# Kernel tuning notes

Measured on AMD Instinct MI355X. Metric: run time of the kernel, lower is better.

Reference implementation:

```python
import jax, jax.numpy as jnp
import numpy as np
from jax.scipy.special import logsumexp

B, S, T = 128, 2048, 64


def setup_inputs() -> dict:
    key = jax.random.key(0)
    k_em, k_tags, k_tr, k_st, k_en = jax.random.split(key, 5)
    emissions = jax.random.normal(k_em, (B, S, T), dtype=jnp.float32)
    tags = jax.random.randint(k_tags, (B, S), 0, T, dtype=jnp.int32)
    mask = jnp.ones((B, S), dtype=jnp.bool_)
    transitions = jax.random.normal(k_tr, (T, T), dtype=jnp.float32)
    start_transitions = jax.random.normal(k_st, (T,), dtype=jnp.float32)
    end_transitions = jax.random.normal(k_en, (T,), dtype=jnp.float32)
    return {"emissions": emissions, "tags": tags, "mask": mask,
            "transitions": transitions, "start_transitions": start_transitions,
            "end_transitions": end_transitions}


def _compute_score(emissions, tags, mask, transitions, start_t, end_t):
    # emissions: (B,S,T), tags: (B,S), mask: (B,S) bool
    maskf = mask.astype(emissions.dtype)
    # emission score at the gold tag per step: (B,S)
    emit = jnp.take_along_axis(emissions, tags[..., None], axis=2)[..., 0]
    # NOTE: source uses transitions[curr_tags, prev_tags]
    trans = transitions[tags[:, 1:], tags[:, :-1]]  # (B,S-1)
    score = start_t[tags[:, 0]] + emit[:, 0]
    score = score + jnp.sum((trans + emit[:, 1:]) * maskf[:, 1:], axis=1)
    last_idx = jnp.sum(mask.astype(jnp.int32), axis=1) - 1  # (B,)
    last_tags = jnp.take_along_axis(tags, last_idx[:, None], axis=1)[:, 0]
    return score + end_t[last_tags]


def _compute_partition(emissions, mask, transitions, end_t, start_t):
    # forward algorithm as a scan; alpha: (B,T)
    alpha0 = start_t + emissions[:, 0]

    def step(alpha, inp):
        em_t, m_t = inp  # (B,T), (B,)
        # next_alpha[b,j] = logsumexp_i alpha[b,i] + transitions[i,j] + em_t[b,j]
        next_alpha = logsumexp(alpha[:, :, None] + transitions[None], axis=1) + em_t
        alpha = jnp.where(m_t[:, None], next_alpha, alpha)
        return alpha, None

    ems = jnp.swapaxes(emissions[:, 1:], 0, 1)  # (S-1,B,T)
    ms = jnp.swapaxes(mask[:, 1:], 0, 1)        # (S-1,B)
    alpha, _ = jax.lax.scan(step, alpha0, (ems, ms))
    return logsumexp(alpha + end_t, axis=1)


def reference(emissions, tags, mask, transitions, start_transitions, end_transitions):
    score = _compute_score(emissions, tags, mask, transitions, start_transitions, end_transitions)
    partition = _compute_partition(emissions, mask, transitions, end_transitions, start_transitions)
    return -(score - partition).mean()
```

## Files before the change

kernel.cpp:

```cpp
#include <hip/hip_runtime.h>
#include <hip/hip_bf16.h>

#define TT 64
#define SS 2048
#define BB 128
#define CC 16
#define LL (SS / CC)
#define PAN 2
#define PCOLS 32
#define CSTRIDE 136

using bf16x8 = __attribute__((ext_vector_type(8))) short;
using f32x4  = __attribute__((ext_vector_type(4))) float;

union B8u { uint4 u; bf16x8 v; };

__device__ __forceinline__ float fexp2(float x) { return __builtin_amdgcn_exp2f(x); }
__device__ __forceinline__ float flog2(float x) { return __builtin_amdgcn_logf(x); }
__device__ __forceinline__ float fexp(float x)  { return fexp2(x * 1.4426950408889634f); }

__device__ __forceinline__ float wave_max(float v) {
#pragma unroll
    for (int off = 32; off > 0; off >>= 1) v = fmaxf(v, __shfl_xor(v, off, 64));
    return v;
}

__device__ __forceinline__ float wave_sum(float v) {
#pragma unroll
    for (int off = 32; off > 0; off >>= 1) v += __shfl_xor(v, off, 64);
    return v;
}

__device__ __forceinline__ unsigned pack_bf16(float lo, float hi) {
    return __builtin_amdgcn_perm(__float_as_uint(hi), __float_as_uint(lo), 0x07060302u);
}

__global__ __launch_bounds__(64, 4) void crf_chunk_kernel(
    const float* __restrict__ emissions,
    const float* __restrict__ transitions,
    __hip_bfloat16* __restrict__ Ms,
    float* __restrict__ Mbase)
{
    const int blk = blockIdx.x;
    const int p = blk & 1;
    const int c = (blk >> 1) & (CC - 1);
    const int b = blk >> 5;
    const int l = threadIdx.x;
    const int c16 = l & 15, q = l >> 4;
    const float LOG2E = 1.4426950408889634f;

    __shared__ __align__(16) unsigned char sbuf[PCOLS * CSTRIDE];
    __shared__ __align__(16) float xbuf[2][TT];

    bf16x8 A[4][2];
#pragma unroll
    for (int mt = 0; mt < 4; ++mt)
#pragma unroll
        for (int kt = 0; kt < 2; ++kt) {
            const int row = mt * 16 + c16;
#pragma unroll
            for (int jj = 0; jj < 8; ++jj) {
                const int k = kt * 32 + q * 8 + jj;
                float e = fexp(transitions[k * TT + row]);
                A[mt][kt][jj] = (short)(__float_as_uint(e) >> 16);
            }
        }

    const int t0 = (c == 0) ? 1 : c * LL;
    const int t1 = c * LL + LL - 1;
    const float* emb = emissions + (size_t)b * SS * TT;

    {
        int* ib = (int*)sbuf;
#pragma unroll
        for (int i = l; i < PCOLS * CSTRIDE / 4; i += 64) ib[i] = 0;
        asm volatile("" ::: "memory");
        if (l < PCOLS)
            *(unsigned short*)(sbuf + l * CSTRIDE + (p * PCOLS + l) * 2) = 0x3F80;
        xbuf[t0 & 1][l] = fexp2(emb[(size_t)t0 * TT + l] * LOG2E);
        asm volatile("" ::: "memory");
    }

    float base = 0.f;

#define CRF_STEP(T, RENORM)                                                   \
    {                                                                         \
        const int tcur = (T);                                                 \
        const int tp = tcur + 1 > t1 ? t1 : tcur + 1;                         \
        float emN = emb[(size_t)tp * TT + l];                                 \
        B8u Bf[2][2];                                           \
        _Pragma("unroll")                                                     \
        for (int kt = 0; kt < 2; ++kt)                                        \
            _Pragma("unroll")                                                 \
            for (int nt = 0; nt < 2; ++nt) {                                  \
                const unsigned char* pb = sbuf + (nt * 16 + c16) * CSTRIDE + kt * 64 + q * 16; \
                uint2 lo = *(const uint2*)pb;                                 \
                uint2 hi = *(const uint2*)(pb + 8);                           \
                Bf[kt][nt].u = make_uint4(lo.x, lo.y, hi.x, hi.y);            \
            }                                                                 \
        f32x4 xvv[4];                                                         \
        _Pragma("unroll")                                                     \
        for (int mt = 0; mt < 4; ++mt)                                        \
            xvv[mt] = *(const f32x4*)&xbuf[tcur & 1][mt * 16 + q * 4];        \
        f32x4 D[4][2];                                                        \
        __builtin_amdgcn_s_setprio(1);                                        \
        _Pragma("unroll")                                                     \
        for (int mt = 0; mt < 4; ++mt)                                        \
            _Pragma("unroll")                                                 \
            for (int nt = 0; nt < 2; ++nt) {                                  \
                f32x4 z = {0.f, 0.f, 0.f, 0.f};                               \
                z = __builtin_amdgcn_mfma_f32_16x16x32_bf16(A[mt][0], Bf[0][nt].v, z, 0, 0, 0); \
                z = __builtin_amdgcn_mfma_f32_16x16x32_bf16(A[mt][1], Bf[1][nt].v, z, 0, 0, 0); \
                D[mt][nt] = z;                                                \
            }                                                                 \
        __builtin_amdgcn_s_setprio(0);                                        \
        xbuf[(tcur + 1) & 1][l] = fexp2(emN * LOG2E);    \
        if (RENORM) {                                                         \
             \
             \
            unsigned mb = (unsigned)__builtin_amdgcn_readfirstlane(           \
                (int)__float_as_uint(D[0][0][0]));                            \
            int e = (int)(mb >> 23) - 126 + 8;                                \
            float s = __uint_as_float((unsigned)(127 - e) << 23);   \
            base += (float)e;                                                 \
            _Pragma("unroll")                                                 \
            for (int mt = 0; mt < 4; ++mt) xvv[mt] *= s;                      \
        }                                                                     \
        _Pragma("unroll")                                                     \
        for (int mt = 0; mt < 4; ++mt)                                        \
            _Pragma("unroll")                                                 \
            for (int nt = 0; nt < 2; ++nt) {                                  \
                f32x4 prod = D[mt][nt] * xvv[mt];                             \
                uint2 w;                                                      \
                w.x = pack_bf16(prod[0], prod[1]);                            \
                w.y = pack_bf16(prod[2], prod[3]);                            \
                *(uint2*)(sbuf + (nt * 16 + c16) * CSTRIDE + mt * 32 + q * 8) = w; \
            }                                                                 \
        asm volatile("" ::: "memory");         \
    }

    int t = t0;
    while (t & 3) {
        CRF_STEP(t, ((t & 3) == 3));
        ++t;
    }
    for (; t <= t1; t += 4) {
        CRF_STEP(t, 0);
        CRF_STEP(t + 1, 0);
        CRF_STEP(t + 2, 0);
        CRF_STEP(t + 3, 1);
    }
#undef CRF_STEP

    {
        unsigned* op = (unsigned*)(Ms + (size_t)blk * 2048 + (size_t)l * PCOLS);
#pragma unroll
        for (int i2 = 0; i2 < 16; ++i2) {
            unsigned short s0 = *(const unsigned short*)(sbuf + (2 * i2) * CSTRIDE + l * 2);
            unsigned short s1 = *(const unsigned short*)(sbuf + (2 * i2 + 1) * CSTRIDE + l * 2);
            op[i2] = (unsigned)s0 | ((unsigned)s1 << 16);
        }
        if (l == 0) Mbase[blk] = base;
    }
}

__global__ __launch_bounds__(256) void crf_fused_tail(
    const float* __restrict__ emissions,
    const int* __restrict__ tags,
    const float* __restrict__ transitions,
    const float* __restrict__ start_t,
    const float* __restrict__ end_t,
    const __hip_bfloat16* __restrict__ Ms,
    const float* __restrict__ Mbase,
    float* __restrict__ out)
{
    const int b = blockIdx.x;
    const int tid = threadIdx.x;
    const int wv = tid >> 6;
    const int j = tid & 63;
    const float LOG2E = 1.4426950408889634f;
    const float LN2   = 0.6931471805599453f;
    __shared__ __align__(16) float pbuf[TT];
    __shared__ float red[4];
    __shared__ float bred[4];

    uint4 m[4 * PAN];
    float bp[PAN];
    {
        const int pbase = (b * CC + wv) * PAN;
        const uint4* src = (const uint4*)(Ms + (size_t)pbase * 2048) + j * 4;
#pragma unroll
        for (int pp = 0; pp < PAN; ++pp) {
#pragma unroll
            for (int d = 0; d < 4; ++d) m[4 * pp + d] = src[pp * 256 + d];
            bp[pp] = Mbase[pbase + pp];
        }
    }

    const int* tg = tags + b * SS;
    const float* em = emissions + (size_t)b * SS * TT;
    {
        const int s0 = tid * 8;
        int4 ta = *(const int4*)(tg + s0);
        int4 tb = *(const int4*)(tg + s0 + 4);
        int t_[8] = {ta.x, ta.y, ta.z, ta.w, tb.x, tb.y, tb.z, tb.w};
        float acc = 0.f;
#pragma unroll
        for (int u = 0; u < 8; ++u) acc += em[(s0 + u) * TT + t_[u]];
#pragma unroll
        for (int u = 1; u < 8; ++u) acc += transitions[t_[u] * TT + t_[u - 1]];
        if (tid > 0) acc += transitions[t_[0] * TT + tg[s0 - 1]];
        if (tid == 0) acc += start_t[t_[0]];
        if (tid == 255) acc += end_t[t_[7]];
        acc = wave_sum(acc);
        if (j == 0) red[wv] = acc;
    }

    float btot = 0.f;
    if (wv == 0) {
        float r2 = (start_t[j] + em[j]) * LOG2E;
        float m2 = wave_max(r2);
        btot = m2;
        pbuf[j] = fexp2(r2 - m2);
    }
    __syncthreads();

    for (int cch = 0; cch < CC; ++cch) {
        if (wv == (cch & 3)) {
            float bmax = fmaxf(bp[0], bp[1]);
            float acc = 0.f;
#pragma unroll
            for (int pp = 0; pp < PAN; ++pp) {
                float dot = 0.f;
#pragma unroll
                for (int d = 0; d < 4; ++d) {
                    uint4 u4 = m[4 * pp + d];
                    const float* pb = pbuf + pp * PCOLS + d * 8;
                    unsigned uu[4] = {u4.x, u4.y, u4.z, u4.w};
#pragma unroll
                    for (int k = 0; k < 4; ++k) {
                        dot = fmaf(__uint_as_float(uu[k] << 16), pb[2 * k], dot);
                        dot = fmaf(__uint_as_float(uu[k] & 0xFFFF0000u), pb[2 * k + 1], dot);
                    }
                }
                acc = fmaf(fexp2(bp[pp] - bmax), dot, acc);
            }
            float mv = wave_max(acc);
            float v = acc / mv;
            btot += bmax + flog2(mv);
            const int nch = cch + 4;
            if (nch < CC) {
                const int pbase = (b * CC + nch) * PAN;
                const uint4* src = (const uint4*)(Ms + (size_t)pbase * 2048) + j * 4;
#pragma unroll
                for (int pp = 0; pp < PAN; ++pp) {
#pragma unroll
                    for (int d = 0; d < 4; ++d) m[4 * pp + d] = src[pp * 256 + d];
                    bp[pp] = Mbase[pbase + pp];
                }
            }
            pbuf[j] = v;
        }
        __syncthreads();
    }

    if (j == 0) bred[wv] = btot;
    __syncthreads();

    if (wv == 0) {
        float v = pbuf[j];
        float w = v * fexp(end_t[j]);
        float s = wave_sum(w);
        if (j == 0) {
            float Btot = (bred[0] + bred[1]) + (bred[2] + bred[3]);
            float partition = LN2 * (Btot + flog2(s));
            float score = (red[0] + red[1]) + (red[2] + red[3]);
            atomicAdd(out, (partition - score) * (1.0f / BB));
        }
    }
}

__global__ __launch_bounds__(256) void crf_score_kernel(
    const float* __restrict__ emissions,
    const int* __restrict__ tags,
    const float* __restrict__ transitions,
    const float* __restrict__ start_t,
    const float* __restrict__ end_t,
    float* __restrict__ score)
{
    const int b = blockIdx.x;
    const int tid = threadIdx.x;
    const int* tg = tags + b * SS;
    const float* em = emissions + (size_t)b * SS * TT;
    const int s0 = tid * 8;
    int4 ta = *(const int4*)(tg + s0);
    int4 tb = *(const int4*)(tg + s0 + 4);
    int t_[8] = {ta.x, ta.y, ta.z, ta.w, tb.x, tb.y, tb.z, tb.w};
    float acc = 0.f;
#pragma unroll
    for (int u = 0; u < 8; ++u) acc += em[(s0 + u) * TT + t_[u]];
#pragma unroll
    for (int u = 1; u < 8; ++u) acc += transitions[t_[u] * TT + t_[u - 1]];
    if (tid > 0) acc += transitions[t_[0] * TT + tg[s0 - 1]];
    if (tid == 0) acc += start_t[t_[0]];
    if (tid == 255) acc += end_t[t_[7]];
    acc = wave_sum(acc);
    __shared__ float red[4];
    if ((tid & 63) == 0) red[tid >> 6] = acc;
    __syncthreads();
    if (tid == 0) score[b] = (red[0] + red[1]) + (red[2] + red[3]);
}

__global__ __launch_bounds__(64, 1) void crf_partition_seq(
    const float* __restrict__ emissions,
    const float* __restrict__ transitions,
    const float* __restrict__ start_t,
    const float* __restrict__ end_t,
    float* __restrict__ partition)
{
    const int b = blockIdx.x;
    const int j = threadIdx.x;
    const float LOG2E = 1.4426950408889634f;
    const float LN2   = 0.6931471805599453f;
    const float* em = emissions + (size_t)b * SS * TT;
    __shared__ __align__(16) float pbuf[TT];

    float E[TT];
#pragma unroll
    for (int k = 0; k < TT; ++k)
        E[k] = fexp2(transitions[k * TT + j] * LOG2E);

    float r = (start_t[j] + em[j]) * LOG2E;
    float base;
    { float m = wave_max(r); base = m; r -= m; }

    for (int t = 1; t < SS; ++t) {
        float emv = em[t * TT + j];
        float p = fexp2(r);
        pbuf[j] = p;
        asm volatile("" ::: "memory");
        float a0 = 0.f, a1 = 0.f, a2 = 0.f, a3 = 0.f;
        const float4* pb4 = (const float4*)pbuf;
#pragma unroll
        for (int cc = 0; cc < 16; ++cc) {
            float4 pv = pb4[cc];
            a0 = fmaf(pv.x, E[4 * cc + 0], a0);
            a1 = fmaf(pv.y, E[4 * cc + 1], a1);
            a2 = fmaf(pv.z, E[4 * cc + 2], a2);
            a3 = fmaf(pv.w, E[4 * cc + 3], a3);
        }
        asm volatile("" ::: "memory");
        r = fmaf(emv, LOG2E, flog2((a0 + a1) + (a2 + a3)));
        if ((t & 3) == 3) { float m = wave_max(r); base += m; r -= m; }
    }
    float v = fmaf(end_t[j], LOG2E, r);
    float m = wave_max(v);
    float s = wave_sum(fexp2(v - m));
    if (j == 0) partition[b] = LN2 * (base + m + flog2(s));
}

__global__ __launch_bounds__(128) void crf_final_kernel(
    const float* __restrict__ partition,
    const float* __restrict__ score,
    float* __restrict__ out)
{
    const int i = threadIdx.x;
    float d = partition[i] - score[i];
#pragma unroll
    for (int off = 32; off > 0; off >>= 1) d += __shfl_xor(d, off, 64);
    __shared__ float red[2];
    if ((i & 63) == 0) red[i >> 6] = d;
    __syncthreads();
    if (i == 0) out[0] = (red[0] + red[1]) * (1.0f / BB);
}

extern "C" void kernel_launch(void* const* d_in, const int* in_sizes, int n_in,
                              void* d_out, int out_size, void* d_ws, size_t ws_size,
                              hipStream_t stream) {
    const float* emissions   = (const float*)d_in[0];
    const int*   tags        = (const int*)d_in[1];
    const float* transitions = (const float*)d_in[3];
    const float* start_t     = (const float*)d_in[4];
    const float* end_t       = (const float*)d_in[5];

    const int NPANEL = BB * CC * PAN;
    const size_t MS_BYTES = (size_t)NPANEL * 2048 * 2;
    unsigned char* w = (unsigned char*)d_ws;
    __hip_bfloat16* Ms = (__hip_bfloat16*)w;
    float* Mbase       = (float*)(w + MS_BYTES);
    const size_t need  = MS_BYTES + NPANEL * sizeof(float);

    if (ws_size >= need) {
        hipMemsetAsync(d_out, 0, sizeof(float), stream);
        crf_chunk_kernel<<<NPANEL, 64, 0, stream>>>(emissions, transitions, Ms, Mbase);
        crf_fused_tail<<<BB, 256, 0, stream>>>(emissions, tags, transitions,
                                               start_t, end_t, Ms, Mbase, (float*)d_out);
    } else {
        float* p2 = (float*)d_ws;
        float* sc = p2 + BB;
        crf_partition_seq<<<BB, 64, 0, stream>>>(emissions, transitions, start_t, end_t, p2);
        crf_score_kernel<<<BB, 256, 0, stream>>>(emissions, tags, transitions, start_t, end_t, sc);
        crf_final_kernel<<<1, 128, 0, stream>>>(p2, sc, (float*)d_out);
    }
}
```

Baseline: 239.5 us.

## Keep chunk transfer-matrix state in MFMA registers instead of LDS round-trip

Switches from 16x16x32 bf16 MFMA to 16x16x16 bf16 MFMA, whose output fragment layout matches the B-operand layout, so the running product stays in registers each step. This removes the per-step LDS write and read of the B panel and the initial LDS zeroing. It doubles the MFMA instruction count per step (narrower K) and adds an f16 fallback path with different renormalisation frequency.

```diff
diff --git a/kernel.cpp b/kernel.cpp
--- a/kernel.cpp
+++ b/kernel.cpp
@@ -1,5 +1,6 @@
 #include <hip/hip_runtime.h>
 #include <hip/hip_bf16.h>
+#include <hip/hip_fp16.h>
 
 #define TT 64
 #define SS 2048
@@ -10,10 +11,9 @@
 #define PCOLS 32
 #define CSTRIDE 136
 
-using bf16x8 = __attribute__((ext_vector_type(8))) short;
+using bf16x4 = __attribute__((ext_vector_type(4))) short;
+using f16x4  = __attribute__((ext_vector_type(4))) _Float16;
 using f32x4  = __attribute__((ext_vector_type(4))) float;
-
-union B8u { uint4 u; bf16x8 v; };
 
 __device__ __forceinline__ float fexp2(float x) { return __builtin_amdgcn_exp2f(x); }
 __device__ __forceinline__ float flog2(float x) { return __builtin_amdgcn_logf(x); }
@@ -34,6 +34,33 @@
 __device__ __forceinline__ unsigned pack_bf16(float lo, float hi) {
     return __builtin_amdgcn_perm(__float_as_uint(hi), __float_as_uint(lo), 0x07060302u);
 }
+
+__device__ __forceinline__ unsigned pack_f16(float lo, float hi) {
+    auto h = __builtin_amdgcn_cvt_pkrtz(lo, hi);
+    union { decltype(h) v; unsigned u; } cv;
+    cv.v = h;
+    return cv.u;
+}
+
+#if !defined(__HIP_DEVICE_COMPILE__) || __has_builtin(__builtin_amdgcn_mfma_f32_16x16x16bf16_1k)
+  #define USE_BF16 1
+  #define RPER 4
+  #define ONE16 0x3F80u
+  typedef bf16x4 abfrag;
+  #define MFMA16(A, B, C) __builtin_amdgcn_mfma_f32_16x16x16bf16_1k((A), (B), (C), 0, 0, 0)
+  #define PK(lo, hi) pack_bf16((lo), (hi))
+#elif __has_builtin(__builtin_amdgcn_mfma_f32_16x16x16f16)
+  #define USE_BF16 0
+  #define RPER 2
+  #define ONE16 0x3C00u
+  typedef f16x4 abfrag;
+  #define MFMA16(A, B, C) __builtin_amdgcn_mfma_f32_16x16x16f16((A), (B), (C), 0, 0, 0)
+  #define PK(lo, hi) pack_f16((lo), (hi))
+#else
+  #error "no 16x16x16 mfma available"
+#endif
+
+union Bu { uint2 u; abfrag v; };
 
 __global__ __launch_bounds__(64, 4) void crf_chunk_kernel(
     const float* __restrict__ emissions,
@@ -52,34 +79,42 @@
     __shared__ __align__(16) unsigned char sbuf[PCOLS * CSTRIDE];
     __shared__ __align__(16) float xbuf[2][TT];
 
-    bf16x8 A[4][2];
+    abfrag A[4][4];
 #pragma unroll
     for (int mt = 0; mt < 4; ++mt)
 #pragma unroll
-        for (int kt = 0; kt < 2; ++kt) {
+        for (int kt = 0; kt < 4; ++kt) {
             const int row = mt * 16 + c16;
 #pragma unroll
-            for (int jj = 0; jj < 8; ++jj) {
-                const int k = kt * 32 + q * 8 + jj;
+            for (int jj = 0; jj < 4; ++jj) {
+                const int k = kt * 16 + q * 4 + jj;
                 float e = fexp(transitions[k * TT + row]);
+#if USE_BF16
                 A[mt][kt][jj] = (short)(__float_as_uint(e) >> 16);
+#else
+                A[mt][kt][jj] = (_Float16)e;
+#endif
             }
+        }
+
+    Bu Bfr[4][2];
+#pragma unroll
+    for (int kt = 0; kt < 4; ++kt)
+#pragma unroll
+        for (int nt = 0; nt < 2; ++nt) {
+            const int gcol = p * 32 + nt * 16 + c16;
+            const int r0 = kt * 16 + q * 4;
+            unsigned d0 = (r0 + 0 == gcol ? ONE16 : 0u) | ((r0 + 1 == gcol ? ONE16 : 0u) << 16);
+            unsigned d1 = (r0 + 2 == gcol ? ONE16 : 0u) | ((r0 + 3 == gcol ? ONE16 : 0u) << 16);
+            Bfr[kt][nt].u = make_uint2(d0, d1);
         }
 
     const int t0 = (c == 0) ? 1 : c * LL;
     const int t1 = c * LL + LL - 1;
     const float* emb = emissions + (size_t)b * SS * TT;
 
-    {
-        int* ib = (int*)sbuf;
-#pragma unroll
-        for (int i = l; i < PCOLS * CSTRIDE / 4; i += 64) ib[i] = 0;
-        asm volatile("" ::: "memory");
-        if (l < PCOLS)
-            *(unsigned short*)(sbuf + l * CSTRIDE + (p * PCOLS + l) * 2) = 0x3F80;
-        xbuf[t0 & 1][l] = fexp2(emb[(size_t)t0 * TT + l] * LOG2E);
-        asm volatile("" ::: "memory");
-    }
+    xbuf[t0 & 1][l] = fexp2(emb[(size_t)t0 * TT + l] * LOG2E);
+    asm volatile("" ::: "memory");
 
     float base = 0.f;
 
@@ -88,16 +123,6 @@
         const int tcur = (T);                                                 \
         const int tp = tcur + 1 > t1 ? t1 : tcur + 1;                         \
         float emN = emb[(size_t)tp * TT + l];                                 \
-        B8u Bf[2][2];                                           \
-        _Pragma("unroll")                                                     \
-        for (int kt = 0; kt < 2; ++kt)                                        \
-            _Pragma("unroll")                                                 \
-            for (int nt = 0; nt < 2; ++nt) {                                  \
-                const unsigned char* pb = sbuf + (nt * 16 + c16) * CSTRIDE + kt * 64 + q * 16; \
-                uint2 lo = *(const uint2*)pb;                                 \
-                uint2 hi = *(const uint2*)(pb + 8);                           \
-                Bf[kt][nt].u = make_uint4(lo.x, lo.y, hi.x, hi.y);            \
-            }                                                                 \
         f32x4 xvv[4];                                                         \
         _Pragma("unroll")                                                     \
         for (int mt = 0; mt < 4; ++mt)                                        \
@@ -109,12 +134,15 @@
             _Pragma("unroll")                                                 \
             for (int nt = 0; nt < 2; ++nt) {                                  \
                 f32x4 z = {0.f, 0.f, 0.f, 0.f};                               \
-                z = __builtin_amdgcn_mfma_f32_16x16x32_bf16(A[mt][0], Bf[0][nt].v, z, 0, 0, 0); \
-                z = __builtin_amdgcn_mfma_f32_16x16x32_bf16(A[mt][1], Bf[1][nt].v, z, 0, 0, 0); \
+                z = MFMA16(A[mt][0], Bfr[0][nt].v, z);                        \
+                z = MFMA16(A[mt][1], Bfr[1][nt].v, z);                        \
+                z = MFMA16(A[mt][2], Bfr[2][nt].v, z);                        \
+                z = MFMA16(A[mt][3], Bfr[3][nt].v, z);                        \
                 D[mt][nt] = z;                                                \
             }                                                                 \
         __builtin_amdgcn_s_setprio(0);                                        \
-        xbuf[(tcur + 1) & 1][l] = fexp2(emN * LOG2E);    \
+        xbuf[(tcur + 1) & 1][l] = fexp2(emN * LOG2E);                         \
+        asm volatile("" ::: "memory");                                        \
         if (RENORM) {                                                         \
              \
              \
@@ -131,28 +159,50 @@
             _Pragma("unroll")                                                 \
             for (int nt = 0; nt < 2; ++nt) {                                  \
                 f32x4 prod = D[mt][nt] * xvv[mt];                             \
-                uint2 w;                                                      \
-                w.x = pack_bf16(prod[0], prod[1]);                            \
-                w.y = pack_bf16(prod[2], prod[3]);                            \
-                *(uint2*)(sbuf + (nt * 16 + c16) * CSTRIDE + mt * 32 + q * 8) = w; \
+                Bfr[mt][nt].u.x = PK(prod[0], prod[1]);                       \
+                Bfr[mt][nt].u.y = PK(prod[2], prod[3]);                       \
             }                                                                 \
-        asm volatile("" ::: "memory");         \
     }
 
     int t = t0;
-    while (t & 3) {
-        CRF_STEP(t, ((t & 3) == 3));
+    while (t & (RPER - 1)) {
+        CRF_STEP(t, ((t & (RPER - 1)) == RPER - 1));
         ++t;
     }
-    for (; t <= t1; t += 4) {
+    for (; t <= t1; t += RPER) {
+#if RPER == 4
         CRF_STEP(t, 0);
         CRF_STEP(t + 1, 0);
         CRF_STEP(t + 2, 0);
         CRF_STEP(t + 3, 1);
+#else
+        CRF_STEP(t, 0);
+        CRF_STEP(t + 1, 1);
+#endif
     }
 #undef CRF_STEP
 
     {
+#pragma unroll
+        for (int kt = 0; kt < 4; ++kt)
+#pragma unroll
+            for (int nt = 0; nt < 2; ++nt) {
+                unsigned d0 = Bfr[kt][nt].u.x;
+                unsigned d1 = Bfr[kt][nt].u.y;
+#if !USE_BF16
+                {
+                    float l0 = __half2float(__ushort_as_half((unsigned short)(d0 & 0xFFFF)));
+                    float h0 = __half2float(__ushort_as_half((unsigned short)(d0 >> 16)));
+                    float l1 = __half2float(__ushort_as_half((unsigned short)(d1 & 0xFFFF)));
+                    float h1 = __half2float(__ushort_as_half((unsigned short)(d1 >> 16)));
+                    d0 = pack_bf16(l0, h0);
+                    d1 = pack_bf16(l1, h1);
+                }
+#endif
+                unsigned char* cbase = sbuf + (nt * 16 + c16) * CSTRIDE + (kt * 16 + q * 4) * 2;
+                *(uint2*)cbase = make_uint2(d0, d1);
+            }
+        asm volatile("" ::: "memory");
         unsigned* op = (unsigned*)(Ms + (size_t)blk * 2048 + (size_t)l * PCOLS);
 #pragma unroll
         for (int i2 = 0; i2 < 16; ++i2) {
@@ -391,7 +441,7 @@
     const size_t need  = MS_BYTES + NPANEL * sizeof(float);
 
     if (ws_size >= need) {
-        hipMemsetAsync(d_out, 0, sizeof(float), stream);
+        (void)hipMemsetAsync(d_out, 0, sizeof(float), stream);
         crf_chunk_kernel<<<NPANEL, 64, 0, stream>>>(emissions, transitions, Ms, Mbase);
         crf_fused_tail<<<BB, 256, 0, stream>>>(emissions, tags, transitions,
                                                start_t, end_t, Ms, Mbase, (float*)d_out);
```

Result: slower. 264.3 us (+10.4%).

## Keep recurrence state in registers using 32x32 MFMA and permlane32 swaps

Applied to the files above, without the earlier changes.

Each chunk step now uses 32x32x16 bf16 MFMAs instead of 16x16x32 ones, with the transition matrix laid out to match. The running product matrix stays in registers as the B operand, and the output-to-input layout change is done with permlane32_swap rather than a round trip through LDS. This removes per-step LDS writes and reads and their latency from the serial dependency chain. The cost is a more intricate lane permutation, including a runtime flip probe, and a shuffle fallback when the builtin is missing.

```diff
diff --git a/kernel.cpp b/kernel.cpp
--- a/kernel.cpp
+++ b/kernel.cpp
@@ -1,5 +1,6 @@
 #include <hip/hip_runtime.h>
 #include <hip/hip_bf16.h>
+#include <hip/hip_fp16.h>
 
 #define TT 64
 #define SS 2048
@@ -9,11 +10,11 @@
 #define PAN 2
 #define PCOLS 32
 #define CSTRIDE 136
+#define RPER 4
 
 using bf16x8 = __attribute__((ext_vector_type(8))) short;
 using f32x4  = __attribute__((ext_vector_type(4))) float;
-
-union B8u { uint4 u; bf16x8 v; };
+using f32x16 = __attribute__((ext_vector_type(16))) float;
 
 __device__ __forceinline__ float fexp2(float x) { return __builtin_amdgcn_exp2f(x); }
 __device__ __forceinline__ float flog2(float x) { return __builtin_amdgcn_logf(x); }
@@ -33,6 +34,40 @@
 
 __device__ __forceinline__ unsigned pack_bf16(float lo, float hi) {
     return __builtin_amdgcn_perm(__float_as_uint(hi), __float_as_uint(lo), 0x07060302u);
+}
+
+#if !defined(__HIP_DEVICE_COMPILE__) || __has_builtin(__builtin_amdgcn_permlane32_swap)
+#define HAVE_PLSWAP 1
+#else
+#define HAVE_PLSWAP 0
+#endif
+
+__device__ __forceinline__ void plswap2(unsigned &x, unsigned &y) {
+#if HAVE_PLSWAP
+    static_assert(sizeof(__builtin_amdgcn_permlane32_swap(0, 0, false, false)) == 8,
+                  "permlane32_swap must return two dwords");
+    auto pr = __builtin_amdgcn_permlane32_swap((int)x, (int)y, false, false);
+    x = (unsigned)((int*)&pr)[0];
+    y = (unsigned)((int*)&pr)[1];
+#else
+    const int h = (int)((threadIdx.x >> 5) & 1);
+    unsigned sx = (unsigned)__shfl_xor((int)x, 32, 64);
+    unsigned sy = (unsigned)__shfl_xor((int)y, 32, 64);
+    unsigned nx = h ? sy : x;
+    unsigned ny = h ? y : sx;
+    x = nx; y = ny;
+#endif
+}
+
+__device__ __forceinline__ int plswap_flip() {
+#if HAVE_PLSWAP
+    int l = (int)threadIdx.x;
+    auto pr = __builtin_amdgcn_permlane32_swap(l, 1000 + l, false, false);
+    int r0 = ((int*)&pr)[0];
+    return (__builtin_amdgcn_readfirstlane(r0) != 0) ? 1 : 0;
+#else
+    return 0;
+#endif
 }
 
 __global__ __launch_bounds__(64, 4) void crf_chunk_kernel(
@@ -46,40 +81,48 @@
     const int c = (blk >> 1) & (CC - 1);
     const int b = blk >> 5;
     const int l = threadIdx.x;
-    const int c16 = l & 15, q = l >> 4;
+    const int n = l & 31;
+    const int h = l >> 5;
     const float LOG2E = 1.4426950408889634f;
 
     __shared__ __align__(16) unsigned char sbuf[PCOLS * CSTRIDE];
     __shared__ __align__(16) float xbuf[2][TT];
 
-    bf16x8 A[4][2];
-#pragma unroll
-    for (int mt = 0; mt < 4; ++mt)
-#pragma unroll
-        for (int kt = 0; kt < 2; ++kt) {
-            const int row = mt * 16 + c16;
+    const int flip = plswap_flip();
+
+    bf16x8 A[2][4];
+#pragma unroll
+    for (int mt = 0; mt < 2; ++mt)
+#pragma unroll
+        for (int kt = 0; kt < 4; ++kt) {
+            const int m = 32 * mt + n;
 #pragma unroll
             for (int jj = 0; jj < 8; ++jj) {
-                const int k = kt * 32 + q * 8 + jj;
-                float e = fexp(transitions[k * TT + row]);
+                const int d = jj >> 1;
+                const int k = 16 * kt + 8 * h + 2 * (d & 1) + 4 * ((d >> 1) ^ flip) + (jj & 1);
+                float e = fexp(transitions[k * TT + m]);
                 A[mt][kt][jj] = (short)(__float_as_uint(e) >> 16);
             }
+        }
+
+    union B8 { unsigned d[4]; bf16x8 v; } S[4];
+#pragma unroll
+    for (int kt = 0; kt < 4; ++kt)
+#pragma unroll
+        for (int d = 0; d < 4; ++d) {
+            const int R = 16 * kt + 8 * h + 2 * (d & 1) + 4 * ((d >> 1) ^ flip);
+            const int gcol = p * 32 + n;
+            unsigned lo = (R == gcol) ? 0x3F80u : 0u;
+            unsigned hi = (R + 1 == gcol) ? 0x3F80u : 0u;
+            S[kt].d[d] = lo | (hi << 16);
         }
 
     const int t0 = (c == 0) ? 1 : c * LL;
     const int t1 = c * LL + LL - 1;
     const float* emb = emissions + (size_t)b * SS * TT;
 
-    {
-        int* ib = (int*)sbuf;
-#pragma unroll
-        for (int i = l; i < PCOLS * CSTRIDE / 4; i += 64) ib[i] = 0;
-        asm volatile("" ::: "memory");
-        if (l < PCOLS)
-            *(unsigned short*)(sbuf + l * CSTRIDE + (p * PCOLS + l) * 2) = 0x3F80;
-        xbuf[t0 & 1][l] = fexp2(emb[(size_t)t0 * TT + l] * LOG2E);
-        asm volatile("" ::: "memory");
-    }
+    xbuf[t0 & 1][l] = fexp2(emb[(size_t)t0 * TT + l] * LOG2E);
+    asm volatile("" ::: "memory");
 
     float base = 0.f;
 
@@ -88,63 +131,64 @@
         const int tcur = (T);                                                 \
         const int tp = tcur + 1 > t1 ? t1 : tcur + 1;                         \
         float emN = emb[(size_t)tp * TT + l];                                 \
-        B8u Bf[2][2];                                           \
-        _Pragma("unroll")                                                     \
-        for (int kt = 0; kt < 2; ++kt)                                        \
-            _Pragma("unroll")                                                 \
-            for (int nt = 0; nt < 2; ++nt) {                                  \
-                const unsigned char* pb = sbuf + (nt * 16 + c16) * CSTRIDE + kt * 64 + q * 16; \
-                uint2 lo = *(const uint2*)pb;                                 \
-                uint2 hi = *(const uint2*)(pb + 8);                           \
-                Bf[kt][nt].u = make_uint4(lo.x, lo.y, hi.x, hi.y);            \
-            }                                                                 \
-        f32x4 xvv[4];                                                         \
-        _Pragma("unroll")                                                     \
-        for (int mt = 0; mt < 4; ++mt)                                        \
-            xvv[mt] = *(const f32x4*)&xbuf[tcur & 1][mt * 16 + q * 4];        \
-        f32x4 D[4][2];                                                        \
+        f32x16 Dt[2];                                                         \
         __builtin_amdgcn_s_setprio(1);                                        \
         _Pragma("unroll")                                                     \
-        for (int mt = 0; mt < 4; ++mt)                                        \
-            _Pragma("unroll")                                                 \
-            for (int nt = 0; nt < 2; ++nt) {                                  \
-                f32x4 z = {0.f, 0.f, 0.f, 0.f};                               \
-                z = __builtin_amdgcn_mfma_f32_16x16x32_bf16(A[mt][0], Bf[0][nt].v, z, 0, 0, 0); \
-                z = __builtin_amdgcn_mfma_f32_16x16x32_bf16(A[mt][1], Bf[1][nt].v, z, 0, 0, 0); \
-                D[mt][nt] = z;                                                \
-            }                                                                 \
+        for (int mt = 0; mt < 2; ++mt) {                                      \
+            f32x16 z = {0.f, 0.f, 0.f, 0.f, 0.f, 0.f, 0.f, 0.f,               \
+                        0.f, 0.f, 0.f, 0.f, 0.f, 0.f, 0.f, 0.f};              \
+            z = __builtin_amdgcn_mfma_f32_32x32x16_bf16(A[mt][0], S[0].v, z, 0, 0, 0); \
+            z = __builtin_amdgcn_mfma_f32_32x32x16_bf16(A[mt][1], S[1].v, z, 0, 0, 0); \
+            z = __builtin_amdgcn_mfma_f32_32x32x16_bf16(A[mt][2], S[2].v, z, 0, 0, 0); \
+            z = __builtin_amdgcn_mfma_f32_32x32x16_bf16(A[mt][3], S[3].v, z, 0, 0, 0); \
+            Dt[mt] = z;                                                       \
+        }                                                                     \
         __builtin_amdgcn_s_setprio(0);                                        \
-        xbuf[(tcur + 1) & 1][l] = fexp2(emN * LOG2E);    \
+        xbuf[(tcur + 1) & 1][l] = fexp2(emN * LOG2E);                         \
+        float sren = 1.f;                                                     \
         if (RENORM) {                                                         \
              \
-             \
             unsigned mb = (unsigned)__builtin_amdgcn_readfirstlane(           \
-                (int)__float_as_uint(D[0][0][0]));                            \
+                (int)__float_as_uint(Dt[0][0]));                              \
             int e = (int)(mb >> 23) - 126 + 8;                                \
-            float s = __uint_as_float((unsigned)(127 - e) << 23);   \
+            sren = __uint_as_float((unsigned)(127 - e) << 23);      \
             base += (float)e;                                                 \
+        }                                                                     \
+        unsigned pd[2][8];                                                    \
+        _Pragma("unroll")                                                     \
+        for (int mt = 0; mt < 2; ++mt)                                        \
             _Pragma("unroll")                                                 \
-            for (int mt = 0; mt < 4; ++mt) xvv[mt] *= s;                      \
+            for (int s4 = 0; s4 < 4; ++s4) {                                  \
+                        \
+                f32x4 xs = *(const f32x4*)&xbuf[tcur & 1][mt * 32 + s4 * 8 + 4 * h]; \
+                if (RENORM) xs *= sren;                                       \
+                float q0 = Dt[mt][4 * s4 + 0] * xs[0];                        \
+                float q1 = Dt[mt][4 * s4 + 1] * xs[1];                        \
+                float q2 = Dt[mt][4 * s4 + 2] * xs[2];                        \
+                float q3 = Dt[mt][4 * s4 + 3] * xs[3];                        \
+                pd[mt][2 * s4]     = pack_bf16(q0, q1);                       \
+                pd[mt][2 * s4 + 1] = pack_bf16(q2, q3);                       \
+            }                                                                 \
+         \
+        _Pragma("unroll")                                                     \
+        for (int kt = 0; kt < 4; ++kt) {                                      \
+            const int ms = kt >> 1;                                           \
+            const int g0 = 4 * (kt & 1);                                      \
+            unsigned a0 = pd[ms][g0 + 0], b0 = pd[ms][g0 + 2];                \
+            unsigned a1 = pd[ms][g0 + 1], b1 = pd[ms][g0 + 3];                \
+            plswap2(a0, b0);                                                  \
+            plswap2(a1, b1);                                                  \
+            S[kt].d[0] = a0; S[kt].d[1] = a1; S[kt].d[2] = b0; S[kt].d[3] = b1; \
         }                                                                     \
-        _Pragma("unroll")                                                     \
-        for (int mt = 0; mt < 4; ++mt)                                        \
-            _Pragma("unroll")                                                 \
-            for (int nt = 0; nt < 2; ++nt) {                                  \
-                f32x4 prod = D[mt][nt] * xvv[mt];                             \
-                uint2 w;                                                      \
-                w.x = pack_bf16(prod[0], prod[1]);                            \
-                w.y = pack_bf16(prod[2], prod[3]);                            \
-                *(uint2*)(sbuf + (nt * 16 + c16) * CSTRIDE + mt * 32 + q * 8) = w; \
-            }                                                                 \
-        asm volatile("" ::: "memory");         \
+        asm volatile("" ::: "memory");                                        \
     }
 
     int t = t0;
-    while (t & 3) {
-        CRF_STEP(t, ((t & 3) == 3));
+    while (t & (RPER - 1)) {
+        CRF_STEP(t, ((t & (RPER - 1)) == RPER - 1));
         ++t;
     }
-    for (; t <= t1; t += 4) {
+    for (; t <= t1; t += RPER) {
         CRF_STEP(t, 0);
         CRF_STEP(t + 1, 0);
         CRF_STEP(t + 2, 0);
@@ -153,6 +197,14 @@
 #undef CRF_STEP
 
     {
+#pragma unroll
+        for (int kt = 0; kt < 4; ++kt) {
+            const int r01 = 16 * kt + 8 * h + 4 * flip;
+            const int r23 = 16 * kt + 8 * h + 4 * (1 - flip);
+            *(uint2*)(sbuf + n * CSTRIDE + r01 * 2) = make_uint2(S[kt].d[0], S[kt].d[1]);
+            *(uint2*)(sbuf + n * CSTRIDE + r23 * 2) = make_uint2(S[kt].d[2], S[kt].d[3]);
+        }
+        asm volatile("" ::: "memory");
         unsigned* op = (unsigned*)(Ms + (size_t)blk * 2048 + (size_t)l * PCOLS);
 #pragma unroll
         for (int i2 = 0; i2 < 16; ++i2) {
@@ -391,7 +443,7 @@
     const size_t need  = MS_BYTES + NPANEL * sizeof(float);
 
     if (ws_size >= need) {
-        hipMemsetAsync(d_out, 0, sizeof(float), stream);
+        (void)hipMemsetAsync(d_out, 0, sizeof(float), stream);
         crf_chunk_kernel<<<NPANEL, 64, 0, stream>>>(emissions, transitions, Ms, Mbase);
         crf_fused_tail<<<BB, 256, 0, stream>>>(emissions, tags, transitions,
                                                start_t, end_t, Ms, Mbase, (float*)d_out);
```

Measured after the change: 231.4 us. 3.4% less time.
